# Kernel tuning notes

Hardware: AMD Instinct MI355X
Metric: run time of the kernel (lower is better)

## Reference

```python
import jax, jax.numpy as jnp
import numpy as np

N = 16384      # nodes
E = 262144     # edges (avg degree 16)
T = 4          # type_num
D = 64         # d_model
L = 2          # layers


def setup_inputs() -> dict:
    key = jax.random.key(0)
    ks = jax.random.split(key, 7)
    return {
        "x": jax.random.normal(ks[0], (N, D), dtype=jnp.float32),
        "edge_feature": jax.random.normal(ks[1], (T, D), dtype=jnp.float32),
        "theta": jax.random.normal(ks[2], (L, T, 3 * D), dtype=jnp.float32) * (1.0 / np.sqrt(3 * D)),
        "wr": jax.random.normal(ks[3], (L, D, D), dtype=jnp.float32) * (1.0 / np.sqrt(D)),
        "we": jax.random.normal(ks[4], (L, D, D), dtype=jnp.float32) * (1.0 / np.sqrt(D)),
        "edge_index": jax.random.randint(ks[5], (2, E), 0, N, dtype=jnp.int64),
        "edge_type": jax.random.randint(ks[6], (E,), 0, T, dtype=jnp.int64),
    }


def _scatter_softmax(r, row, num_nodes):
    # r: [T, E]; softmax over edges grouped by destination node `row`.
    rT = r.T  # [E, T] (segment ops reduce over leading axis)
    m = jax.ops.segment_max(rT, row, num_segments=num_nodes)   # [N, T]
    e = jnp.exp(rT - m[row])                                    # [E, T]
    s = jax.ops.segment_sum(e, row, num_segments=num_nodes)     # [N, T]
    return (e / s[row]).T                                       # [T, E]


def reference(x, edge_feature, theta, wr, we, edge_index, edge_type):
    n, d = x.shape
    t = edge_feature.shape[0]
    num_layers = theta.shape[0]
    row, col = edge_index[0], edge_index[1]

    h = jnp.broadcast_to(x[None], (t, n, d))  # x.expand(type_num, N, d)
    ef = edge_feature                          # [T, D]
    for i in range(num_layers):
        tg, thi, thj = theta[i, :, :d], theta[i, :, d:2 * d], theta[i, :, 2 * d:]
        # per-edge scores
        r_g = (tg @ ef.T)[:, edge_type]                        # [T, E]
        r_hi = jnp.einsum('tnd,td->tn', h, thi)[:, row]        # [T, E]
        r_hj = jnp.einsum('tnd,td->tn', h, thj)[:, col]        # [T, E]
        r = _scatter_softmax(r_g + r_hi + r_hj, row, n)        # [T, E]
        # gated messages
        ef = ef @ wr[i]                                        # [T, D]
        v_g = jax.nn.sigmoid(ef)[edge_type]                    # [E, D]
        v_h = jnp.einsum('tnd,de->tne', h, we[i])[:, col]      # [T, E, D]
        msg = r[:, :, None] * v_g[None] * v_h                  # [T, E, D]
        agg = jax.ops.segment_sum(jnp.moveaxis(msg, 1, 0), row, num_segments=n)  # [N, T, D]
        h = jnp.moveaxis(agg, 0, 1)                            # [T, N, D]
        if i < num_layers - 1:
            h = jax.nn.relu(h)      # dropout is identity in eval mode
            ef = jax.nn.relu(ef)
    return h
```

## Files before the change

### kernel.cpp

```cpp
#include <hip/hip_runtime.h>

#define NN 16384
#define EE 262144
#define TT 4
#define DD 64
#define SLOT 96
#define HB (EE / 256)
#define NB (NN / 64)

__device__ inline float wave_reduce_max(float v) {
    #pragma unroll
    for (int off = 32; off >= 1; off >>= 1) v = fmaxf(v, __shfl_xor(v, off));
    return v;
}
__device__ inline float wave_reduce_sum(float v) {
    #pragma unroll
    for (int off = 32; off >= 1; off >>= 1) v += __shfl_xor(v, off);
    return v;
}
__device__ inline float4 edge_group_reduce(float4 v) {
    #pragma unroll
    for (int off = 16; off < 64; off <<= 1) {
        v.x += __shfl_xor(v.x, off); v.y += __shfl_xor(v.y, off);
        v.z += __shfl_xor(v.z, off); v.w += __shfl_xor(v.w, off);
    }
    return v;
}
__device__ inline unsigned short f2bf(float f) {
    unsigned u = __float_as_uint(f);
    u += 0x7FFFu + ((u >> 16) & 1u);
    return (unsigned short)(u >> 16);
}
__device__ inline float bf2f(unsigned short h) {
    return __uint_as_float(((unsigned)h) << 16);
}
__device__ inline float4 bf4_to_f4(ushort4 h) {
    return float4{bf2f(h.x), bf2f(h.y), bf2f(h.z), bf2f(h.w)};
}

#define ONL(mm, ss, r) { if ((r) > (mm)) { ss = ss * __expf(mm - (r)) + 1.f; mm = (r); } \
                         else ss += __expf((r) - (mm)); }

__global__ __launch_bounds__(256) void build_node0_kernel(
        const int* __restrict__ row, const int* __restrict__ col,
        const int* __restrict__ et, int* __restrict__ cnt,
        int* __restrict__ ce_slot,
        const float* __restrict__ x, const float* __restrict__ theta,
        const float* __restrict__ we, const float* __restrict__ ef_in,
        const float* __restrict__ wr,
        float* __restrict__ a4, float* __restrict__ b4,
        unsigned short* __restrict__ hw0,
        float* __restrict__ sg, float* __restrict__ rg) {
    __shared__ float h_lds[64][68];
    __shared__ float4 we_lds[64][16];
    __shared__ float th_lds[4][2][64];
    __shared__ float part_a[64][4][4];
    __shared__ float part_b[64][4][4];
    __shared__ float ef0[TT * DD];
    __shared__ float ef1[TT * DD];
    int tid = threadIdx.x;
    int bid = blockIdx.x;

    if (bid < HB) {
        int e = bid * 256 + tid;
        int r = row[e];
        int pos = atomicAdd(&cnt[r], 1);
        if (pos < SLOT)
            ce_slot[r * SLOT + pos] = col[e] | (et[e] << 14);
        return;
    }
    bid -= HB;

    if (bid == NB) {
        int t = tid >> 6, d = tid & 63;
        ef0[tid] = ef_in[tid];
        __syncthreads();
        if (tid < 16) {
            int tt = tid & 3, tq = tid >> 2;
            float s = 0.f;
            for (int k = 0; k < DD; ++k) s += theta[tq * 192 + k] * ef0[tt * DD + k];
            rg[tq * 4 + tt] = s;
        }
        float acc = 0.f;
        for (int k = 0; k < DD; ++k) acc += ef0[t * DD + k] * wr[k * DD + d];
        sg[tid] = 1.f / (1.f + __expf(-acc));
        ef1[tid] = fmaxf(acc, 0.f);
        __syncthreads();
        if (tid < 16) {
            int tt = tid & 3, tq = tid >> 2;
            float s = 0.f;
            for (int k = 0; k < DD; ++k) s += theta[(TT + tq) * 192 + k] * ef1[tt * DD + k];
            rg[16 + tq * 4 + tt] = s;
        }
        float acc2 = 0.f;
        for (int k = 0; k < DD; ++k) acc2 += ef1[t * DD + k] * wr[DD * DD + k * DD + d];
        sg[TT * DD + tid] = 1.f / (1.f + __expf(-acc2));
        return;
    }

    int n0 = bid * 64;
    {
        int q = tid & 15, nr = tid >> 4;
        #pragma unroll
        for (int r = 0; r < 4; ++r) {
            int n = r * 16 + nr;
            *(float4*)&h_lds[n][4 * q] = ((const float4*)x)[(n0 + n) * 16 + q];
        }
    }
    {
        const float4* we4 = (const float4*)we;
        #pragma unroll
        for (int r = 0; r < 4; ++r)
            ((float4*)we_lds)[tid + 256 * r] = we4[tid + 256 * r];
    }
    {
        #pragma unroll
        for (int r = 0; r < 2; ++r) {
            int e = tid + 256 * r;
            int t = e >> 7, ab = (e >> 6) & 1, k = e & 63;
            th_lds[t][ab][k] = theta[t * 192 + 64 + ab * 64 + k];
        }
    }
    __syncthreads();
    int i = tid >> 4, j = tid & 15;
    float4 acc[4];
    acc[0] = acc[1] = acc[2] = acc[3] = float4{0.f, 0.f, 0.f, 0.f};
    for (int k = 0; k < 64; ++k) {
        float4 wv = we_lds[k][j];
        #pragma unroll
        for (int r = 0; r < 4; ++r) {
            float hv = h_lds[4 * i + r][k];
            acc[r].x += hv * wv.x; acc[r].y += hv * wv.y;
            acc[r].z += hv * wv.z; acc[r].w += hv * wv.w;
        }
    }
    {
        int t = j >> 2, kq = j & 3;
        float pa[4] = {0, 0, 0, 0}, pb[4] = {0, 0, 0, 0};
        for (int kk = 0; kk < 16; ++kk) {
            int k = kq * 16 + kk;
            float ti = th_lds[t][0][k], tj = th_lds[t][1][k];
            #pragma unroll
            for (int r = 0; r < 4; ++r) {
                float hv = h_lds[4 * i + r][k];
                pa[r] += hv * ti; pb[r] += hv * tj;
            }
        }
        #pragma unroll
        for (int r = 0; r < 4; ++r) {
            part_a[4 * i + r][t][kq] = pa[r];
            part_b[4 * i + r][t][kq] = pb[r];
        }
    }
    #pragma unroll
    for (int r = 0; r < 4; ++r) {
        ushort4 hv;
        hv.x = f2bf(acc[r].x); hv.y = f2bf(acc[r].y);
        hv.z = f2bf(acc[r].z); hv.w = f2bf(acc[r].w);
        ((ushort4*)hw0)[(n0 + 4 * i + r) * 16 + j] = hv;
    }
    __syncthreads();
    {
        int n = tid >> 2, t = tid & 3;
        float4 va = *(float4*)&part_a[n][t][0];
        float4 vb = *(float4*)&part_b[n][t][0];
        a4[(n0 + n) * 4 + t] = va.x + va.y + va.z + va.w;
        b4[(n0 + n) * 4 + t] = vb.x + vb.y + vb.z + vb.w;
    }
}

__global__ __launch_bounds__(256) void node1_kernel(
        const float* __restrict__ h1, const float* __restrict__ theta,
        const float* __restrict__ we,
        float* __restrict__ a4, float* __restrict__ b4,
        unsigned short* __restrict__ hw) {
    __shared__ float h_lds[64][68];
    __shared__ float4 we_lds[64][16];
    __shared__ float th_lds[2][64];
    __shared__ float part_a[64][17];
    __shared__ float part_b[64][17];
    int tid = threadIdx.x;
    int t = blockIdx.y;
    int n0 = blockIdx.x * 64;
    const float* ht = h1 + (size_t)t * NN * DD;
    {
        int q = tid & 15, nr = tid >> 4;
        #pragma unroll
        for (int r = 0; r < 4; ++r) {
            int n = r * 16 + nr;
            *(float4*)&h_lds[n][4 * q] = ((const float4*)ht)[(n0 + n) * 16 + q];
        }
    }
    {
        const float4* we4 = (const float4*)(we + DD * DD);
        #pragma unroll
        for (int r = 0; r < 4; ++r)
            ((float4*)we_lds)[tid + 256 * r] = we4[tid + 256 * r];
    }
    if (tid < 128) {
        int ab = tid >> 6, k = tid & 63;
        th_lds[ab][k] = theta[(TT + t) * 192 + 64 + ab * 64 + k];
    }
    __syncthreads();
    int i = tid >> 4, j = tid & 15;
    float4 acc[4];
    acc[0] = acc[1] = acc[2] = acc[3] = float4{0.f, 0.f, 0.f, 0.f};
    for (int k = 0; k < 64; ++k) {
        float4 wv = we_lds[k][j];
        #pragma unroll
        for (int r = 0; r < 4; ++r) {
            float hv = h_lds[4 * i + r][k];
            acc[r].x += hv * wv.x; acc[r].y += hv * wv.y;
            acc[r].z += hv * wv.z; acc[r].w += hv * wv.w;
        }
    }
    {
        float pa[4] = {0, 0, 0, 0}, pb[4] = {0, 0, 0, 0};
        #pragma unroll
        for (int kk = 0; kk < 4; ++kk) {
            int k = 4 * j + kk;
            float ti = th_lds[0][k], tj = th_lds[1][k];
            #pragma unroll
            for (int r = 0; r < 4; ++r) {
                float hv = h_lds[4 * i + r][k];
                pa[r] += hv * ti; pb[r] += hv * tj;
            }
        }
        #pragma unroll
        for (int r = 0; r < 4; ++r) {
            part_a[4 * i + r][j] = pa[r];
            part_b[4 * i + r][j] = pb[r];
        }
    }
    #pragma unroll
    for (int r = 0; r < 4; ++r) {
        ushort4 hv;
        hv.x = f2bf(acc[r].x); hv.y = f2bf(acc[r].y);
        hv.z = f2bf(acc[r].z); hv.w = f2bf(acc[r].w);
        ((ushort4*)hw)[((size_t)t * NN + n0 + 4 * i + r) * 16 + j] = hv;
    }
    __syncthreads();
    if (tid < 64) {
        float s = 0.f;
        #pragma unroll
        for (int jj = 0; jj < 16; ++jj) s += part_a[tid][jj];
        a4[(n0 + tid) * 4 + t] = s;
    } else if (tid < 128) {
        int n = tid - 64;
        float s = 0.f;
        #pragma unroll
        for (int jj = 0; jj < 16; ++jj) s += part_b[n][jj];
        b4[(n0 + n) * 4 + t] = s;
    }
}

__global__ __launch_bounds__(256) void edge_agg0_kernel(
        const int* __restrict__ cnt, const int* __restrict__ ce_slot,
        const float* __restrict__ a4, const float* __restrict__ b4,
        const float* __restrict__ rg, const float* __restrict__ sg,
        const unsigned short* __restrict__ hw0, float* __restrict__ h1) {
    __shared__ float4 sg4[64];
    __shared__ float4 rg4[4];
    __shared__ int cols[4][SLOT];
    __shared__ float4 wT[4][SLOT];
    int tid = threadIdx.x;
    if (tid < 64) sg4[tid] = ((const float4*)sg)[tid];
    if (tid < 4)  rg4[tid] = float4{rg[tid], rg[4 + tid], rg[8 + tid], rg[12 + tid]};
    int w = tid >> 6, lane = tid & 63;
    int n = blockIdx.x * 4 + w;
    int deg = cnt[n]; if (deg > SLOT) deg = SLOT;
    const int* ces = ce_slot + n * SLOT;
    float4 av = ((const float4*)a4)[n];
    __syncthreads();

    float m0 = -INFINITY, m1 = -INFINITY, m2 = -INFINITY, m3 = -INFINITY;
    float s0 = 0.f, s1 = 0.f, s2 = 0.f, s3 = 0.f;
    for (int e = lane; e < deg; e += 64) {
        int pk = ces[e];
        int c = pk & 16383, tt = pk >> 14;
        float4 bv = ((const float4*)b4)[c];
        float4 rv = rg4[tt];
        float4 rp{av.x + bv.x + rv.x, av.y + bv.y + rv.y,
                  av.z + bv.z + rv.z, av.w + bv.w + rv.w};
        cols[w][e] = pk;
        wT[w][e] = rp;
        ONL(m0, s0, rp.x) ONL(m1, s1, rp.y) ONL(m2, s2, rp.z) ONL(m3, s3, rp.w)
    }
    float M0 = wave_reduce_max(m0), M1 = wave_reduce_max(m1);
    float M2 = wave_reduce_max(m2), M3 = wave_reduce_max(m3);
    float S0 = wave_reduce_sum((m0 > -INFINITY) ? s0 * __expf(m0 - M0) : 0.f);
    float S1 = wave_reduce_sum((m1 > -INFINITY) ? s1 * __expf(m1 - M1) : 0.f);
    float S2 = wave_reduce_sum((m2 > -INFINITY) ? s2 * __expf(m2 - M2) : 0.f);
    float S3 = wave_reduce_sum((m3 > -INFINITY) ? s3 * __expf(m3 - M3) : 0.f);
    float i0 = (S0 > 0.f) ? 1.f / S0 : 0.f, i1 = (S1 > 0.f) ? 1.f / S1 : 0.f;
    float i2 = (S2 > 0.f) ? 1.f / S2 : 0.f, i3 = (S3 > 0.f) ? 1.f / S3 : 0.f;
    for (int e = lane; e < deg; e += 64) {
        float4 rp = wT[w][e];
        wT[w][e] = float4{__expf(rp.x - M0) * i0, __expf(rp.y - M1) * i1,
                          __expf(rp.z - M2) * i2, __expf(rp.w - M3) * i3};
    }

    int eg = lane >> 4, q = lane & 15;
    float4 acc0{0,0,0,0}, acc1{0,0,0,0}, acc2{0,0,0,0}, acc3{0,0,0,0};
    const ushort4* hw4 = (const ushort4*)hw0;
    for (int base = 0; base < deg; base += 4) {
        int e = base + eg;
        if (e < deg) {
            int pk = cols[w][e];
            int c = pk & 16383, tt = pk >> 14;
            ushort4 hv = hw4[c * 16 + q];
            float4 sgv = sg4[tt * 16 + q];
            float4 wv = wT[w][e];
            float4 f = bf4_to_f4(hv);
            float4 g{sgv.x * f.x, sgv.y * f.y, sgv.z * f.z, sgv.w * f.w};
            acc0.x += wv.x * g.x; acc0.y += wv.x * g.y; acc0.z += wv.x * g.z; acc0.w += wv.x * g.w;
            acc1.x += wv.y * g.x; acc1.y += wv.y * g.y; acc1.z += wv.y * g.z; acc1.w += wv.y * g.w;
            acc2.x += wv.z * g.x; acc2.y += wv.z * g.y; acc2.z += wv.z * g.z; acc2.w += wv.z * g.w;
            acc3.x += wv.w * g.x; acc3.y += wv.w * g.y; acc3.z += wv.w * g.z; acc3.w += wv.w * g.w;
        }
    }
    acc0 = edge_group_reduce(acc0);
    acc1 = edge_group_reduce(acc1);
    acc2 = edge_group_reduce(acc2);
    acc3 = edge_group_reduce(acc3);
    float4 o = acc0;
    if (eg == 1) o = acc1;
    if (eg == 2) o = acc2;
    if (eg == 3) o = acc3;
    o.x = fmaxf(o.x, 0.f); o.y = fmaxf(o.y, 0.f);
    o.z = fmaxf(o.z, 0.f); o.w = fmaxf(o.w, 0.f);
    ((float4*)h1)[(eg * NN + n) * 16 + q] = o;
}

__global__ __launch_bounds__(256) void edge_agg1_kernel(
        const int* __restrict__ cnt, const int* __restrict__ ce_slot,
        const float* __restrict__ a4, const float* __restrict__ b4,
        const float* __restrict__ rg, const float* __restrict__ sg,
        const unsigned short* __restrict__ hw, float* __restrict__ out) {
    __shared__ float4 sg4[64];
    __shared__ float4 rg4[4];
    __shared__ int cols[4][SLOT];
    __shared__ float4 wT[4][SLOT];
    int tid = threadIdx.x;
    if (tid < 64) sg4[tid] = ((const float4*)sg)[tid];
    if (tid < 4)  rg4[tid] = float4{rg[tid], rg[4 + tid], rg[8 + tid], rg[12 + tid]};
    int w = tid >> 6, lane = tid & 63;
    int n = blockIdx.x * 4 + w;
    int deg = cnt[n]; if (deg > SLOT) deg = SLOT;
    const int* ces = ce_slot + n * SLOT;
    float4 av = ((const float4*)a4)[n];
    __syncthreads();

    float m0 = -INFINITY, m1 = -INFINITY, m2 = -INFINITY, m3 = -INFINITY;
    float s0 = 0.f, s1 = 0.f, s2 = 0.f, s3 = 0.f;
    for (int e = lane; e < deg; e += 64) {
        int pk = ces[e];
        int c = pk & 16383, tt = pk >> 14;
        float4 bv = ((const float4*)b4)[c];
        float4 rv = rg4[tt];
        float4 rp{av.x + bv.x + rv.x, av.y + bv.y + rv.y,
                  av.z + bv.z + rv.z, av.w + bv.w + rv.w};
        cols[w][e] = pk;
        wT[w][e] = rp;
        ONL(m0, s0, rp.x) ONL(m1, s1, rp.y) ONL(m2, s2, rp.z) ONL(m3, s3, rp.w)
    }
    float M0 = wave_reduce_max(m0), M1 = wave_reduce_max(m1);
    float M2 = wave_reduce_max(m2), M3 = wave_reduce_max(m3);
    float S0 = wave_reduce_sum((m0 > -INFINITY) ? s0 * __expf(m0 - M0) : 0.f);
    float S1 = wave_reduce_sum((m1 > -INFINITY) ? s1 * __expf(m1 - M1) : 0.f);
    float S2 = wave_reduce_sum((m2 > -INFINITY) ? s2 * __expf(m2 - M2) : 0.f);
    float S3 = wave_reduce_sum((m3 > -INFINITY) ? s3 * __expf(m3 - M3) : 0.f);
    float i0 = (S0 > 0.f) ? 1.f / S0 : 0.f, i1 = (S1 > 0.f) ? 1.f / S1 : 0.f;
    float i2 = (S2 > 0.f) ? 1.f / S2 : 0.f, i3 = (S3 > 0.f) ? 1.f / S3 : 0.f;
    for (int e = lane; e < deg; e += 64) {
        float4 rp = wT[w][e];
        wT[w][e] = float4{__expf(rp.x - M0) * i0, __expf(rp.y - M1) * i1,
                          __expf(rp.z - M2) * i2, __expf(rp.w - M3) * i3};
    }

    int eg = lane >> 4, q = lane & 15;
    float4 acc0{0,0,0,0}, acc1{0,0,0,0}, acc2{0,0,0,0}, acc3{0,0,0,0};
    const ushort4* hw4 = (const ushort4*)hw;
    for (int base = 0; base < deg; base += 4) {
        int e = base + eg;
        if (e < deg) {
            int pk = cols[w][e];
            int c = pk & 16383, tt = pk >> 14;
            int ba = c * 16 + q;
            ushort4 h0 = hw4[ba];
            ushort4 h1v = hw4[NN * 16 + ba];
            ushort4 h2 = hw4[2 * NN * 16 + ba];
            ushort4 h3 = hw4[3 * NN * 16 + ba];
            float4 sgv = sg4[tt * 16 + q];
            float4 wv = wT[w][e];
            float4 f0 = bf4_to_f4(h0), f1 = bf4_to_f4(h1v);
            float4 f2 = bf4_to_f4(h2), f3 = bf4_to_f4(h3);
            acc0.x += wv.x * sgv.x * f0.x; acc0.y += wv.x * sgv.y * f0.y;
            acc0.z += wv.x * sgv.z * f0.z; acc0.w += wv.x * sgv.w * f0.w;
            acc1.x += wv.y * sgv.x * f1.x; acc1.y += wv.y * sgv.y * f1.y;
            acc1.z += wv.y * sgv.z * f1.z; acc1.w += wv.y * sgv.w * f1.w;
            acc2.x += wv.z * sgv.x * f2.x; acc2.y += wv.z * sgv.y * f2.y;
            acc2.z += wv.z * sgv.z * f2.z; acc2.w += wv.z * sgv.w * f2.w;
            acc3.x += wv.w * sgv.x * f3.x; acc3.y += wv.w * sgv.y * f3.y;
            acc3.z += wv.w * sgv.z * f3.z; acc3.w += wv.w * sgv.w * f3.w;
        }
    }
    acc0 = edge_group_reduce(acc0);
    acc1 = edge_group_reduce(acc1);
    acc2 = edge_group_reduce(acc2);
    acc3 = edge_group_reduce(acc3);
    float4 o = acc0;
    if (eg == 1) o = acc1;
    if (eg == 2) o = acc2;
    if (eg == 3) o = acc3;
    ((float4*)out)[(eg * NN + n) * 16 + q] = o;
}

extern "C" void kernel_launch(void* const* d_in, const int* in_sizes, int n_in,
                              void* d_out, int out_size, void* d_ws, size_t ws_size,
                              hipStream_t stream) {
    const float* x     = (const float*)d_in[0];
    const float* ef_in = (const float*)d_in[1];
    const float* theta = (const float*)d_in[2];
    const float* wr    = (const float*)d_in[3];
    const float* we    = (const float*)d_in[4];
    const int* edge_index = (const int*)d_in[5];
    const int* edge_type  = (const int*)d_in[6];
    float* out = (float*)d_out;

    const int* row = edge_index;
    const int* col = edge_index + EE;

    char* p = (char*)d_ws;
    auto alloc = [&](size_t bytes) { void* r = (void*)p; p += (bytes + 255) & ~(size_t)255; return r; };
    int*   cnt     = (int*)  alloc((size_t)NN * 4);
    int*   ce_slot = (int*)  alloc((size_t)NN * SLOT * 4);
    float* a4_0    = (float*)alloc((size_t)NN * 4 * 4);
    float* b4_0    = (float*)alloc((size_t)NN * 4 * 4);
    float* a4_1    = (float*)alloc((size_t)NN * 4 * 4);
    float* b4_1    = (float*)alloc((size_t)NN * 4 * 4);
    unsigned short* hw0 = (unsigned short*)alloc((size_t)NN * DD * 2);
    unsigned short* hw1 = (unsigned short*)alloc((size_t)TT * NN * DD * 2);
    float* h1      = (float*)alloc((size_t)TT * NN * DD * 4);
    float* sg      = (float*)alloc((size_t)2 * TT * DD * 4);
    float* rg      = (float*)alloc((size_t)2 * 16 * 4);

    hipMemsetAsync(cnt, 0, (size_t)NN * 4, stream);
    build_node0_kernel<<<HB + NB + 1, 256, 0, stream>>>(
        row, col, edge_type, cnt, ce_slot, x, theta, we, ef_in, wr,
        a4_0, b4_0, hw0, sg, rg);
    edge_agg0_kernel<<<NN / 4, 256, 0, stream>>>(
        cnt, ce_slot, a4_0, b4_0, rg, sg, hw0, h1);
    node1_kernel<<<dim3(NN / 64, TT), 256, 0, stream>>>(
        h1, theta, we, a4_1, b4_1, hw1);
    edge_agg1_kernel<<<NN / 4, 256, 0, stream>>>(
        cnt, ce_slot, a4_1, b4_1, rg + 16, sg + TT * DD, hw1, out);
}
```

Measured before the change: 147.4 us.

## Drop softmax max pass, store h1 in bf16, interleave hw1 per node

Replaces the online max/sum softmax with direct clamped exponentials, so the normalisation happens once after accumulation and the max reduction and second LDS pass go away. The intermediate h1 is stored in bf16 instead of fp32, halving that write and the read in node1. The layer-1 hw buffer is laid out node-major with all four types adjacent, and edge_agg1 now loops over every edge with each 16-lane group handling one type, which removes the cross-group reduction. The exp clamping at ±60 and the bf16 storage of h1 change numerics and can overflow or lose precision for extreme scores.

```diff
diff --git a/kernel.cpp b/kernel.cpp
--- a/kernel.cpp
+++ b/kernel.cpp
@@ -7,12 +7,8 @@
 #define SLOT 96
 #define HB (EE / 256)
 #define NB (NN / 64)
-
-__device__ inline float wave_reduce_max(float v) {
-    #pragma unroll
-    for (int off = 32; off >= 1; off >>= 1) v = fmaxf(v, __shfl_xor(v, off));
-    return v;
-}
+#define WPAD 100
+
 __device__ inline float wave_reduce_sum(float v) {
     #pragma unroll
     for (int off = 32; off >= 1; off >>= 1) v += __shfl_xor(v, off);
@@ -37,9 +33,12 @@
 __device__ inline float4 bf4_to_f4(ushort4 h) {
     return float4{bf2f(h.x), bf2f(h.y), bf2f(h.z), bf2f(h.w)};
 }
-
-#define ONL(mm, ss, r) { if ((r) > (mm)) { ss = ss * __expf(mm - (r)) + 1.f; mm = (r); } \
-                         else ss += __expf((r) - (mm)); }
+__device__ inline ushort4 f4_to_bf4(float4 f) {
+    return ushort4{f2bf(f.x), f2bf(f.y), f2bf(f.z), f2bf(f.w)};
+}
+__device__ inline float cexp(float r) {
+    return __expf(fminf(fmaxf(r, -60.f), 60.f));
+}
 
 __global__ __launch_bounds__(256) void build_node0_kernel(
         const int* __restrict__ row, const int* __restrict__ col,
@@ -153,12 +152,8 @@
         }
     }
     #pragma unroll
-    for (int r = 0; r < 4; ++r) {
-        ushort4 hv;
-        hv.x = f2bf(acc[r].x); hv.y = f2bf(acc[r].y);
-        hv.z = f2bf(acc[r].z); hv.w = f2bf(acc[r].w);
-        ((ushort4*)hw0)[(n0 + 4 * i + r) * 16 + j] = hv;
-    }
+    for (int r = 0; r < 4; ++r)
+        ((ushort4*)hw0)[(n0 + 4 * i + r) * 16 + j] = f4_to_bf4(acc[r]);
     __syncthreads();
     {
         int n = tid >> 2, t = tid & 3;
@@ -170,7 +165,7 @@
 }
 
 __global__ __launch_bounds__(256) void node1_kernel(
-        const float* __restrict__ h1, const float* __restrict__ theta,
+        const unsigned short* __restrict__ h1, const float* __restrict__ theta,
         const float* __restrict__ we,
         float* __restrict__ a4, float* __restrict__ b4,
         unsigned short* __restrict__ hw) {
@@ -182,13 +177,13 @@
     int tid = threadIdx.x;
     int t = blockIdx.y;
     int n0 = blockIdx.x * 64;
-    const float* ht = h1 + (size_t)t * NN * DD;
+    const ushort4* ht = (const ushort4*)h1 + (size_t)t * NN * 16;
     {
         int q = tid & 15, nr = tid >> 4;
         #pragma unroll
         for (int r = 0; r < 4; ++r) {
             int n = r * 16 + nr;
-            *(float4*)&h_lds[n][4 * q] = ((const float4*)ht)[(n0 + n) * 16 + q];
+            *(float4*)&h_lds[n][4 * q] = bf4_to_f4(ht[(n0 + n) * 16 + q]);
         }
     }
     {
@@ -233,12 +228,8 @@
         }
     }
     #pragma unroll
-    for (int r = 0; r < 4; ++r) {
-        ushort4 hv;
-        hv.x = f2bf(acc[r].x); hv.y = f2bf(acc[r].y);
-        hv.z = f2bf(acc[r].z); hv.w = f2bf(acc[r].w);
-        ((ushort4*)hw)[((size_t)t * NN + n0 + 4 * i + r) * 16 + j] = hv;
-    }
+    for (int r = 0; r < 4; ++r)
+        ((ushort4*)hw)[(size_t)(n0 + 4 * i + r) * 64 + t * 16 + j] = f4_to_bf4(acc[r]);
     __syncthreads();
     if (tid < 64) {
         float s = 0.f;
@@ -258,11 +249,11 @@
         const int* __restrict__ cnt, const int* __restrict__ ce_slot,
         const float* __restrict__ a4, const float* __restrict__ b4,
         const float* __restrict__ rg, const float* __restrict__ sg,
-        const unsigned short* __restrict__ hw0, float* __restrict__ h1) {
+        const unsigned short* __restrict__ hw0, unsigned short* __restrict__ h1) {
     __shared__ float4 sg4[64];
     __shared__ float4 rg4[4];
-    __shared__ int cols[4][SLOT];
-    __shared__ float4 wT[4][SLOT];
+    __shared__ int   pkS[4][WPAD];
+    __shared__ float wS[4][4][WPAD];
     int tid = threadIdx.x;
     if (tid < 64) sg4[tid] = ((const float4*)sg)[tid];
     if (tid < 4)  rg4[tid] = float4{rg[tid], rg[4 + tid], rg[8 + tid], rg[12 + tid]};
@@ -273,31 +264,35 @@
     float4 av = ((const float4*)a4)[n];
     __syncthreads();
 
-    float m0 = -INFINITY, m1 = -INFINITY, m2 = -INFINITY, m3 = -INFINITY;
-    float s0 = 0.f, s1 = 0.f, s2 = 0.f, s3 = 0.f;
-    for (int e = lane; e < deg; e += 64) {
-        int pk = ces[e];
-        int c = pk & 16383, tt = pk >> 14;
-        float4 bv = ((const float4*)b4)[c];
-        float4 rv = rg4[tt];
-        float4 rp{av.x + bv.x + rv.x, av.y + bv.y + rv.y,
-                  av.z + bv.z + rv.z, av.w + bv.w + rv.w};
-        cols[w][e] = pk;
-        wT[w][e] = rp;
-        ONL(m0, s0, rp.x) ONL(m1, s1, rp.y) ONL(m2, s2, rp.z) ONL(m3, s3, rp.w)
-    }
-    float M0 = wave_reduce_max(m0), M1 = wave_reduce_max(m1);
-    float M2 = wave_reduce_max(m2), M3 = wave_reduce_max(m3);
-    float S0 = wave_reduce_sum((m0 > -INFINITY) ? s0 * __expf(m0 - M0) : 0.f);
-    float S1 = wave_reduce_sum((m1 > -INFINITY) ? s1 * __expf(m1 - M1) : 0.f);
-    float S2 = wave_reduce_sum((m2 > -INFINITY) ? s2 * __expf(m2 - M2) : 0.f);
-    float S3 = wave_reduce_sum((m3 > -INFINITY) ? s3 * __expf(m3 - M3) : 0.f);
-    float i0 = (S0 > 0.f) ? 1.f / S0 : 0.f, i1 = (S1 > 0.f) ? 1.f / S1 : 0.f;
-    float i2 = (S2 > 0.f) ? 1.f / S2 : 0.f, i3 = (S3 > 0.f) ? 1.f / S3 : 0.f;
-    for (int e = lane; e < deg; e += 64) {
-        float4 rp = wT[w][e];
-        wT[w][e] = float4{__expf(rp.x - M0) * i0, __expf(rp.y - M1) * i1,
-                          __expf(rp.z - M2) * i2, __expf(rp.w - M3) * i3};
+    bool ok1 = lane < deg;
+    int pk1 = ok1 ? ces[lane] : 0;
+    int c1 = pk1 & 16383, tt1 = pk1 >> 14;
+    float4 bv = ((const float4*)b4)[c1];
+    float4 rv = rg4[tt1];
+    float4 w1;
+    w1.x = ok1 ? cexp(av.x + bv.x + rv.x) : 0.f;
+    w1.y = ok1 ? cexp(av.y + bv.y + rv.y) : 0.f;
+    w1.z = ok1 ? cexp(av.z + bv.z + rv.z) : 0.f;
+    w1.w = ok1 ? cexp(av.w + bv.w + rv.w) : 0.f;
+    pkS[w][lane] = pk1;
+    wS[w][0][lane] = w1.x; wS[w][1][lane] = w1.y;
+    wS[w][2][lane] = w1.z; wS[w][3][lane] = w1.w;
+    float4 w2{0.f, 0.f, 0.f, 0.f};
+    if (deg > 64) {
+        bool ok2 = lane + 64 < deg;
+        int pk2 = ok2 ? ces[lane + 64] : 0;
+        int c2 = pk2 & 16383, tt2 = pk2 >> 14;
+        float4 bv2 = ((const float4*)b4)[c2];
+        float4 rv2 = rg4[tt2];
+        w2.x = ok2 ? cexp(av.x + bv2.x + rv2.x) : 0.f;
+        w2.y = ok2 ? cexp(av.y + bv2.y + rv2.y) : 0.f;
+        w2.z = ok2 ? cexp(av.z + bv2.z + rv2.z) : 0.f;
+        w2.w = ok2 ? cexp(av.w + bv2.w + rv2.w) : 0.f;
+        if (lane < WPAD - 64) {
+            pkS[w][64 + lane] = pk2;
+            wS[w][0][64 + lane] = w2.x; wS[w][1][64 + lane] = w2.y;
+            wS[w][2][64 + lane] = w2.z; wS[w][3][64 + lane] = w2.w;
+        }
     }
 
     int eg = lane >> 4, q = lane & 15;
@@ -305,20 +300,25 @@
     const ushort4* hw4 = (const ushort4*)hw0;
     for (int base = 0; base < deg; base += 4) {
         int e = base + eg;
-        if (e < deg) {
-            int pk = cols[w][e];
-            int c = pk & 16383, tt = pk >> 14;
-            ushort4 hv = hw4[c * 16 + q];
-            float4 sgv = sg4[tt * 16 + q];
-            float4 wv = wT[w][e];
-            float4 f = bf4_to_f4(hv);
-            float4 g{sgv.x * f.x, sgv.y * f.y, sgv.z * f.z, sgv.w * f.w};
-            acc0.x += wv.x * g.x; acc0.y += wv.x * g.y; acc0.z += wv.x * g.z; acc0.w += wv.x * g.w;
-            acc1.x += wv.y * g.x; acc1.y += wv.y * g.y; acc1.z += wv.y * g.z; acc1.w += wv.y * g.w;
-            acc2.x += wv.z * g.x; acc2.y += wv.z * g.y; acc2.z += wv.z * g.z; acc2.w += wv.z * g.w;
-            acc3.x += wv.w * g.x; acc3.y += wv.w * g.y; acc3.z += wv.w * g.z; acc3.w += wv.w * g.w;
-        }
-    }
+        int pk = pkS[w][e];
+        int c = pk & 16383, tt = pk >> 14;
+        ushort4 hv = hw4[c * 16 + q];
+        float4 sgv = sg4[tt * 16 + q];
+        float we0 = wS[w][0][e], we1 = wS[w][1][e];
+        float we2 = wS[w][2][e], we3 = wS[w][3][e];
+        float4 f = bf4_to_f4(hv);
+        float4 g{sgv.x * f.x, sgv.y * f.y, sgv.z * f.z, sgv.w * f.w};
+        acc0.x += we0 * g.x; acc0.y += we0 * g.y; acc0.z += we0 * g.z; acc0.w += we0 * g.w;
+        acc1.x += we1 * g.x; acc1.y += we1 * g.y; acc1.z += we1 * g.z; acc1.w += we1 * g.w;
+        acc2.x += we2 * g.x; acc2.y += we2 * g.y; acc2.z += we2 * g.z; acc2.w += we2 * g.w;
+        acc3.x += we3 * g.x; acc3.y += we3 * g.y; acc3.z += we3 * g.z; acc3.w += we3 * g.w;
+    }
+    float S0 = wave_reduce_sum(w1.x + w2.x);
+    float S1 = wave_reduce_sum(w1.y + w2.y);
+    float S2 = wave_reduce_sum(w1.z + w2.z);
+    float S3 = wave_reduce_sum(w1.w + w2.w);
+    float i0 = (S0 > 0.f) ? 1.f / S0 : 0.f, i1 = (S1 > 0.f) ? 1.f / S1 : 0.f;
+    float i2 = (S2 > 0.f) ? 1.f / S2 : 0.f, i3 = (S3 > 0.f) ? 1.f / S3 : 0.f;
     acc0 = edge_group_reduce(acc0);
     acc1 = edge_group_reduce(acc1);
     acc2 = edge_group_reduce(acc2);
@@ -327,9 +327,10 @@
     if (eg == 1) o = acc1;
     if (eg == 2) o = acc2;
     if (eg == 3) o = acc3;
-    o.x = fmaxf(o.x, 0.f); o.y = fmaxf(o.y, 0.f);
-    o.z = fmaxf(o.z, 0.f); o.w = fmaxf(o.w, 0.f);
-    ((float4*)h1)[(eg * NN + n) * 16 + q] = o;
+    float is = (eg == 0) ? i0 : (eg == 1) ? i1 : (eg == 2) ? i2 : i3;
+    o.x = fmaxf(o.x * is, 0.f); o.y = fmaxf(o.y * is, 0.f);
+    o.z = fmaxf(o.z * is, 0.f); o.w = fmaxf(o.w * is, 0.f);
+    ((ushort4*)h1)[(eg * NN + n) * 16 + q] = f4_to_bf4(o);
 }
 
 __global__ __launch_bounds__(256) void edge_agg1_kernel(
@@ -339,8 +340,8 @@
         const unsigned short* __restrict__ hw, float* __restrict__ out) {
     __shared__ float4 sg4[64];
     __shared__ float4 rg4[4];
-    __shared__ int cols[4][SLOT];
-    __shared__ float4 wT[4][SLOT];
+    __shared__ int   pkS[4][WPAD];
+    __shared__ float wS[4][4][WPAD];
     int tid = threadIdx.x;
     if (tid < 64) sg4[tid] = ((const float4*)sg)[tid];
     if (tid < 4)  rg4[tid] = float4{rg[tid], rg[4 + tid], rg[8 + tid], rg[12 + tid]};
@@ -351,69 +352,59 @@
     float4 av = ((const float4*)a4)[n];
     __syncthreads();
 
-    float m0 = -INFINITY, m1 = -INFINITY, m2 = -INFINITY, m3 = -INFINITY;
-    float s0 = 0.f, s1 = 0.f, s2 = 0.f, s3 = 0.f;
-    for (int e = lane; e < deg; e += 64) {
-        int pk = ces[e];
+    bool ok1 = lane < deg;
+    int pk1 = ok1 ? ces[lane] : 0;
+    int c1 = pk1 & 16383, tt1 = pk1 >> 14;
+    float4 bv = ((const float4*)b4)[c1];
+    float4 rv = rg4[tt1];
+    float4 w1;
+    w1.x = ok1 ? cexp(av.x + bv.x + rv.x) : 0.f;
+    w1.y = ok1 ? cexp(av.y + bv.y + rv.y) : 0.f;
+    w1.z = ok1 ? cexp(av.z + bv.z + rv.z) : 0.f;
+    w1.w = ok1 ? cexp(av.w + bv.w + rv.w) : 0.f;
+    pkS[w][lane] = pk1;
+    wS[w][0][lane] = w1.x; wS[w][1][lane] = w1.y;
+    wS[w][2][lane] = w1.z; wS[w][3][lane] = w1.w;
+    float4 w2{0.f, 0.f, 0.f, 0.f};
+    if (deg > 64) {
+        bool ok2 = lane + 64 < deg;
+        int pk2 = ok2 ? ces[lane + 64] : 0;
+        int c2 = pk2 & 16383, tt2 = pk2 >> 14;
+        float4 bv2 = ((const float4*)b4)[c2];
+        float4 rv2 = rg4[tt2];
+        w2.x = ok2 ? cexp(av.x + bv2.x + rv2.x) : 0.f;
+        w2.y = ok2 ? cexp(av.y + bv2.y + rv2.y) : 0.f;
+        w2.z = ok2 ? cexp(av.z + bv2.z + rv2.z) : 0.f;
+        w2.w = ok2 ? cexp(av.w + bv2.w + rv2.w) : 0.f;
+        if (lane < WPAD - 64) {
+            pkS[w][64 + lane] = pk2;
+            wS[w][0][64 + lane] = w2.x; wS[w][1][64 + lane] = w2.y;
+            wS[w][2][64 + lane] = w2.z; wS[w][3][64 + lane] = w2.w;
+        }
+    }
+
+    int eg = lane >> 4, q = lane & 15;
+    float4 acc{0, 0, 0, 0};
+    const ushort4* hw4 = (const ushort4*)hw;
+    for (int e = 0; e < deg; ++e) {
+        int pk = pkS[w][e];
         int c = pk & 16383, tt = pk >> 14;
-        float4 bv = ((const float4*)b4)[c];
-        float4 rv = rg4[tt];
-        float4 rp{av.x + bv.x + rv.x, av.y + bv.y + rv.y,
-                  av.z + bv.z + rv.z, av.w + bv.w + rv.w};
-        cols[w][e] = pk;
-        wT[w][e] = rp;
-        ONL(m0, s0, rp.x) ONL(m1, s1, rp.y) ONL(m2, s2, rp.z) ONL(m3, s3, rp.w)
-    }
-    float M0 = wave_reduce_max(m0), M1 = wave_reduce_max(m1);
-    float M2 = wave_reduce_max(m2), M3 = wave_reduce_max(m3);
-    float S0 = wave_reduce_sum((m0 > -INFINITY) ? s0 * __expf(m0 - M0) : 0.f);
-    float S1 = wave_reduce_sum((m1 > -INFINITY) ? s1 * __expf(m1 - M1) : 0.f);
-    float S2 = wave_reduce_sum((m2 > -INFINITY) ? s2 * __expf(m2 - M2) : 0.f);
-    float S3 = wave_reduce_sum((m3 > -INFINITY) ? s3 * __expf(m3 - M3) : 0.f);
+        ushort4 hv = hw4[c * 64 + eg * 16 + q];
+        float4 sgv = sg4[tt * 16 + q];
+        float wv = wS[w][eg][e];
+        float4 f = bf4_to_f4(hv);
+        acc.x += wv * (sgv.x * f.x); acc.y += wv * (sgv.y * f.y);
+        acc.z += wv * (sgv.z * f.z); acc.w += wv * (sgv.w * f.w);
+    }
+    float S0 = wave_reduce_sum(w1.x + w2.x);
+    float S1 = wave_reduce_sum(w1.y + w2.y);
+    float S2 = wave_reduce_sum(w1.z + w2.z);
+    float S3 = wave_reduce_sum(w1.w + w2.w);
     float i0 = (S0 > 0.f) ? 1.f / S0 : 0.f, i1 = (S1 > 0.f) ? 1.f / S1 : 0.f;
     float i2 = (S2 > 0.f) ? 1.f / S2 : 0.f, i3 = (S3 > 0.f) ? 1.f / S3 : 0.f;
-    for (int e = lane; e < deg; e += 64) {
-        float4 rp = wT[w][e];
-        wT[w][e] = float4{__expf(rp.x - M0) * i0, __expf(rp.y - M1) * i1,
-                          __expf(rp.z - M2) * i2, __expf(rp.w - M3) * i3};
-    }
-
-    int eg = lane >> 4, q = lane & 15;
-    float4 acc0{0,0,0,0}, acc1{0,0,0,0}, acc2{0,0,0,0}, acc3{0,0,0,0};
-    const ushort4* hw4 = (const ushort4*)hw;
-    for (int base = 0; base < deg; base += 4) {
-        int e = base + eg;
-        if (e < deg) {
-            int pk = cols[w][e];
-            int c = pk & 16383, tt = pk >> 14;
-            int ba = c * 16 + q;
-            ushort4 h0 = hw4[ba];
-            ushort4 h1v = hw4[NN * 16 + ba];
-            ushort4 h2 = hw4[2 * NN * 16 + ba];
-            ushort4 h3 = hw4[3 * NN * 16 + ba];
-            float4 sgv = sg4[tt * 16 + q];
-            float4 wv = wT[w][e];
-            float4 f0 = bf4_to_f4(h0), f1 = bf4_to_f4(h1v);
-            float4 f2 = bf4_to_f4(h2), f3 = bf4_to_f4(h3);
-            acc0.x += wv.x * sgv.x * f0.x; acc0.y += wv.x * sgv.y * f0.y;
-            acc0.z += wv.x * sgv.z * f0.z; acc0.w += wv.x * sgv.w * f0.w;
-            acc1.x += wv.y * sgv.x * f1.x; acc1.y += wv.y * sgv.y * f1.y;
-            acc1.z += wv.y * sgv.z * f1.z; acc1.w += wv.y * sgv.w * f1.w;
-            acc2.x += wv.z * sgv.x * f2.x; acc2.y += wv.z * sgv.y * f2.y;
-            acc2.z += wv.z * sgv.z * f2.z; acc2.w += wv.z * sgv.w * f2.w;
-            acc3.x += wv.w * sgv.x * f3.x; acc3.y += wv.w * sgv.y * f3.y;
-            acc3.z += wv.w * sgv.z * f3.z; acc3.w += wv.w * sgv.w * f3.w;
-        }
-    }
-    acc0 = edge_group_reduce(acc0);
-    acc1 = edge_group_reduce(acc1);
-    acc2 = edge_group_reduce(acc2);
-    acc3 = edge_group_reduce(acc3);
-    float4 o = acc0;
-    if (eg == 1) o = acc1;
-    if (eg == 2) o = acc2;
-    if (eg == 3) o = acc3;
-    ((float4*)out)[(eg * NN + n) * 16 + q] = o;
+    float is = (eg == 0) ? i0 : (eg == 1) ? i1 : (eg == 2) ? i2 : i3;
+    acc.x *= is; acc.y *= is; acc.z *= is; acc.w *= is;
+    ((float4*)out)[(eg * NN + n) * 16 + q] = acc;
 }
 
 extern "C" void kernel_launch(void* const* d_in, const int* in_sizes, int n_in,
@@ -441,7 +432,7 @@
     float* b4_1    = (float*)alloc((size_t)NN * 4 * 4);
     unsigned short* hw0 = (unsigned short*)alloc((size_t)NN * DD * 2);
     unsigned short* hw1 = (unsigned short*)alloc((size_t)TT * NN * DD * 2);
-    float* h1      = (float*)alloc((size_t)TT * NN * DD * 4);
+    unsigned short* h1  = (unsigned short*)alloc((size_t)TT * NN * DD * 2);
     float* sg      = (float*)alloc((size_t)2 * TT * DD * 4);
     float* rg      = (float*)alloc((size_t)2 * 16 * 4);
 
```

Measured after the change: 142.9 us (median of 2 runs). 1.03x faster.
